# Kernel tuning notes

Hardware: AMD Instinct MI355X
Metric: run time of the kernel (lower is better)

## Reference

```python
import jax, jax.numpy as jnp
import numpy as np


def setup_inputs() -> dict:
    key = jax.random.key(0)
    ks = jax.random.split(key, 7)
    B, Q, K, H, D, R = 2, 2048, 2048, 16, 64, 32
    queries = jax.random.normal(ks[0], (B, Q, H, D), dtype=jnp.float32)
    keys = jax.random.normal(ks[1], (B, K, H, D), dtype=jnp.float32)
    values = jax.random.normal(ks[2], (B, K, H, D), dtype=jnp.float32)
    att_mask = jax.random.randint(ks[3], (B, Q, K), 0, 2, dtype=jnp.int32)
    relative_att_ids = jax.random.randint(ks[4], (B, Q, K), 0, R, dtype=jnp.int32)
    # TruncatedNormal(stddev=0.5) approximated by clipped normal
    relative_emb_table = jnp.clip(
        0.5 * jax.random.normal(ks[5], (R, H, D), dtype=jnp.float32), -1.0, 1.0)
    relative_bias_table = jnp.zeros((R, H), dtype=jnp.float32)
    return {
        'queries': queries,
        'keys': keys,
        'values': values,
        'att_mask': att_mask,
        'relative_att_ids': relative_att_ids,
        'relative_emb_table': relative_emb_table,
        'relative_bias_table': relative_bias_table,
    }


def reference(queries, keys, values, att_mask, relative_att_ids,
              relative_emb_table, relative_bias_table):
    # content scores: [B,Q,K,H]
    content = jnp.einsum('bqhd,bkhd->bqkh', queries, keys)
    # relative scores per vocab id: [B,Q,R,H]
    all_rel = jnp.einsum('bqhd,rhd->bqrh', queries, relative_emb_table)
    all_rel = all_rel + relative_bias_table  # broadcast [R,H]
    # gather along vocab axis per (q,k): [B,Q,K,H]
    rel = jnp.take_along_axis(
        all_rel, relative_att_ids[:, :, :, None].astype(jnp.int32), axis=2)
    scores = content + rel
    d = queries.shape[-1]
    scores = scores / jnp.sqrt(jnp.asarray(d, scores.dtype))
    mask_adder = -10000.0 * (1.0 - att_mask[:, :, :, None].astype(scores.dtype))
    scores = scores + mask_adder
    probs = jax.nn.softmax(scores, axis=-2)  # softmax over key axis
    return jnp.einsum('bqkh,bkhd->bqhd', probs, values)
```

## Files before the change

### kernel.cpp

```cpp
#include <hip/hip_runtime.h>
#include <hip/hip_fp16.h>
#include <stdint.h>

#define Bn 2
#define Qn 2048
#define Kn 2048
#define Hn 16
#define Dn 64
#define Rn 32

#define LOG2E_8 0.18033688011112042f
#define MASK_NEG -14426.950408889634f

typedef __attribute__((ext_vector_type(8))) short short8v;
typedef __attribute__((ext_vector_type(4))) float f32x4;
typedef __attribute__((ext_vector_type(4))) uint32_t u32x4;

static __device__ __forceinline__ uint16_t bf16rn(float f) {
  uint32_t u = __builtin_bit_cast(uint32_t, f);
  u += 0x7FFFu + ((u >> 16) & 1u);
  return (uint16_t)(u >> 16);
}
static __device__ __forceinline__ float bf16f(uint16_t h) {
  return __builtin_bit_cast(float, (uint32_t)h << 16);
}
static __device__ __forceinline__ float exp2a(float x) {
  float r; asm("v_exp_f32 %0, %1" : "=v"(r) : "v"(x)); return r;
}
static __device__ __forceinline__ uint32_t cvtpk(float lo, float hi) {
  uint32_t r; asm("v_cvt_pk_bf16_f32 %0, %1, %2" : "=v"(r) : "v"(lo), "v"(hi)); return r;
}
static __device__ __forceinline__ void gl_lds16(const void* g, void* l) {
  __builtin_amdgcn_global_load_lds((const __attribute__((address_space(1))) void*)g,
                                   (__attribute__((address_space(3))) void*)l, 16, 0, 0);
}

__global__ void pack_kernel(const int* __restrict__ ids,
                            const int* __restrict__ msk,
                            uint32_t* __restrict__ outp, int n4) {
  int i = blockIdx.x * 256 + threadIdx.x;
  if (i >= n4) return;
  int4 a = reinterpret_cast<const int4*>(ids)[i];
  int4 m = reinterpret_cast<const int4*>(msk)[i];
  uint32_t v = (uint32_t)((a.x | (m.x << 5)) & 0x3f)
             | ((uint32_t)((a.y | (m.y << 5)) & 0x3f) << 8)
             | ((uint32_t)((a.z | (m.z << 5)) & 0x3f) << 16)
             | ((uint32_t)((a.w | (m.w << 5)) & 0x3f) << 24);
  outp[i] = v;
}

__global__ __launch_bounds__(256) void kfrag6_kernel(const float* __restrict__ Kg,
                                                     const float* __restrict__ Vg,
                                                     uint8_t* __restrict__ frag) {
  const int bid = blockIdx.x;
  const int c = bid & 63;
  const int h = (bid >> 6) & 15;
  const int b = bid >> 10;
  uint8_t* panel = frag + (size_t)(b * 16 + h) * 524288u + (size_t)c * 8192u;
  uint4* kf = reinterpret_cast<uint4*>(panel);
  uint4* vf = reinterpret_cast<uint4*>(panel + 4096);
  const int tid = threadIdx.x;
  const int sdq = tid & 7, srow = (tid >> 3) & 15, stile = tid >> 7;
  const int sg = sdq & 3, sdm = sdq >> 2;
  const float* kp = Kg + ((((size_t)b * Kn) + c * 32 + stile * 16 + srow) * Hn + h) * Dn + (sdm * 32 + sg * 4);
  const float4 x0 = *reinterpret_cast<const float4*>(kp);
  const float4 x1 = *reinterpret_cast<const float4*>(kp + 16);
  const float xs0[4] = {x0.x * LOG2E_8, x0.y * LOG2E_8, x0.z * LOG2E_8, x0.w * LOG2E_8};
  const float xs1[4] = {x1.x * LOG2E_8, x1.y * LOG2E_8, x1.z * LOG2E_8, x1.w * LOG2E_8};
  uint4 uh;
  uh.x = bf16rn(xs0[0]) | ((uint32_t)bf16rn(xs0[1]) << 16);
  uh.y = bf16rn(xs0[2]) | ((uint32_t)bf16rn(xs0[3]) << 16);
  uh.z = bf16rn(xs1[0]) | ((uint32_t)bf16rn(xs1[1]) << 16);
  uh.w = bf16rn(xs1[2]) | ((uint32_t)bf16rn(xs1[3]) << 16);
  kf[(stile * 2 + sdm) * 64 + (srow + 16 * sg)] = uh;
  const int vd = tid & 63, vkq = tid >> 6;
  const float* vp = Vg + ((((size_t)b * Kn) + c * 32 + vkq * 4) * Hn + h) * Dn + vd;
  float v0[4], v1[4];
#pragma unroll
  for (int i = 0; i < 4; ++i) {
    v0[i] = vp[i * (Hn * Dn)];
    v1[i] = vp[(16 + i) * (Hn * Dn)];
  }
  uint4 uv;
  uv.x = bf16rn(v0[0]) | ((uint32_t)bf16rn(v0[1]) << 16);
  uv.y = bf16rn(v0[2]) | ((uint32_t)bf16rn(v0[3]) << 16);
  uv.z = bf16rn(v1[0]) | ((uint32_t)bf16rn(v1[1]) << 16);
  uv.w = bf16rn(v1[2]) | ((uint32_t)bf16rn(v1[3]) << 16);
  vf[(vd >> 4) * 64 + (vd & 15) + 16 * vkq] = uv;
}

__global__ __launch_bounds__(256) void tab2_kernel(const float* __restrict__ Qg,
                                                   const float* __restrict__ Eg,
                                                   const float* __restrict__ biasg,
                                                   __half* __restrict__ tabg) {
  const int tid = threadIdx.x;
  const int lane = tid & 63;
  const int w = tid >> 6;
  const int qr = lane & 15;
  const int g = lane >> 4;
  const int bid = blockIdx.x;
  const int qt = bid & 31;
  const int h = (bid >> 5) & 15;
  const int b = bid >> 9;
  const int q0 = qt * 64 + w * 16;

  short8v eh[2][2], el[2][2];
#pragma unroll
  for (int rt = 0; rt < 2; ++rt)
#pragma unroll
    for (int dm = 0; dm < 2; ++dm) {
      const float* ep = Eg + (((size_t)(rt * 16 + qr) * Hn + h) * Dn) + dm * 32 + 4 * g;
      const float4 x0 = *reinterpret_cast<const float4*>(ep);
      const float4 x1 = *reinterpret_cast<const float4*>(ep + 16);
      const float xs[8] = {x0.x * LOG2E_8, x0.y * LOG2E_8, x0.z * LOG2E_8, x0.w * LOG2E_8,
                           x1.x * LOG2E_8, x1.y * LOG2E_8, x1.z * LOG2E_8, x1.w * LOG2E_8};
#pragma unroll
      for (int j = 0; j < 8; ++j) {
        const uint16_t hi = bf16rn(xs[j]);
        eh[rt][dm][j] = (short)hi;
        el[rt][dm][j] = (short)bf16rn(xs[j] - bf16f(hi));
      }
    }
  short8v qh[2], ql[2];
#pragma unroll
  for (int dm = 0; dm < 2; ++dm) {
    const float* qp = Qg + (((size_t)b * Qn + q0 + qr) * Hn + h) * Dn + dm * 32 + 4 * g;
    const float4 x0 = *reinterpret_cast<const float4*>(qp);
    const float4 x1 = *reinterpret_cast<const float4*>(qp + 16);
    const float xs[8] = {x0.x, x0.y, x0.z, x0.w, x1.x, x1.y, x1.z, x1.w};
#pragma unroll
    for (int j = 0; j < 8; ++j) {
      const uint16_t hi = bf16rn(xs[j]);
      qh[dm][j] = (short)hi;
      ql[dm][j] = (short)bf16rn(xs[j] - bf16f(hi));
    }
  }
#pragma unroll
  for (int rt = 0; rt < 2; ++rt) {
    f32x4 d;
#pragma unroll
    for (int j = 0; j < 4; ++j)
      d[j] = LOG2E_8 * biasg[(rt * 16 + 4 * g + j) * Hn + h];
#pragma unroll
    for (int dm = 0; dm < 2; ++dm) {
      d = __builtin_amdgcn_mfma_f32_16x16x32_bf16(eh[rt][dm], qh[dm], d, 0, 0, 0);
      d = __builtin_amdgcn_mfma_f32_16x16x32_bf16(el[rt][dm], qh[dm], d, 0, 0, 0);
      d = __builtin_amdgcn_mfma_f32_16x16x32_bf16(eh[rt][dm], ql[dm], d, 0, 0, 0);
    }
    const size_t rowo = ((size_t)(b * 16 + h) * 2048 + q0 + qr) * 64;
    union { ushort4 u4; __half hh[4]; } um, uu;
#pragma unroll
    for (int j = 0; j < 4; ++j) {
      um.hh[j] = __float2half(d[j] + MASK_NEG);
      uu.hh[j] = __float2half(d[j]);
    }
    *reinterpret_cast<ushort4*>(&tabg[rowo + rt * 16 + 4 * g]) = um.u4;
    *reinterpret_cast<ushort4*>(&tabg[rowo + 32 + rt * 16 + 4 * g]) = uu.u4;
  }
}

__global__ __launch_bounds__(512, 4) void attn9_kernel(
    const float* __restrict__ Qg, const uint8_t* __restrict__ packed,
    const uint8_t* __restrict__ kfragp, const __half* __restrict__ tabg,
    float* __restrict__ outg) {
  __shared__ alignas(16) char smem[65536];
  const int tid = threadIdx.x;
  const int lane = tid & 63;
  const int w = tid >> 6;
  const int w4 = w & 3;
  const int ks = w >> 2;
  const int qr = lane & 15;
  const int g = lane >> 4;

  const int wi = (blockIdx.x & 7) * 64 + (blockIdx.x >> 3);
  const int qt = wi & 15;
  const int h = (wi >> 4) & 15;
  const int b = wi >> 8;
  const int q0 = qt * 128;

  char* const myhalf = smem + 16384 + ks * 24576;
  char* bA = myhalf;
  char* bB = myhalf + 8192;
  char* bC = myhalf + 16384;

  int64_t prow[2];
  int trow[2];
#pragma unroll
  for (int t = 0; t < 2; ++t) {
    prow[t] = ((int64_t)(b * Qn + q0 + w4 * 32 + t * 16 + qr)) * Kn + ks * 1024 + 4 * g;
    trow[t] = (w4 * 32 + t * 16 + qr) * 64;
  }
  uint32_t pc[2][2], pn[2][2] = {{0u, 0u}, {0u, 0u}};
#pragma unroll
  for (int t = 0; t < 2; ++t)
#pragma unroll
    for (int st = 0; st < 2; ++st)
      pc[t][st] = *reinterpret_cast<const uint32_t*>(packed + prow[t] + st * 16);

  {
    const uint8_t* tsrc = reinterpret_cast<const uint8_t*>(
        tabg + ((size_t)(b * 16 + h) * 2048 + q0) * 64);
    char* ld = smem + w * 2048;
    gl_lds16(tsrc + (size_t)w * 2048 + (size_t)lane * 16, ld);
    gl_lds16(tsrc + (size_t)w * 2048 + 1024 + (size_t)lane * 16, ld + 1024);
  }
  const uint8_t* sbase = kfragp + (size_t)(b * 16 + h) * 524288u +
                         (size_t)(ks * 32) * 8192u + (size_t)w4 * 2048 + (size_t)lane * 16;
  {
    char* ld0 = bA + w4 * 2048;
    gl_lds16(sbase, ld0);
    gl_lds16(sbase + 1024, ld0 + 1024);
    char* ld1 = bB + w4 * 2048;
    gl_lds16(sbase + 8192, ld1);
    gl_lds16(sbase + 8192 + 1024, ld1 + 1024);
  }

  short8v qhi[2][2];
#pragma unroll
  for (int t = 0; t < 2; ++t)
#pragma unroll
    for (int dm = 0; dm < 2; ++dm) {
      const float* qp = Qg + (((size_t)b * Qn + q0 + w4 * 32 + t * 16 + qr) * Hn + h) * Dn +
                        dm * 32 + 4 * g;
      const float4 x0 = *reinterpret_cast<const float4*>(qp);
      const float4 x1 = *reinterpret_cast<const float4*>(qp + 16);
      u32x4 u;
      u[0] = cvtpk(x0.x, x0.y); u[1] = cvtpk(x0.z, x0.w);
      u[2] = cvtpk(x1.x, x1.y); u[3] = cvtpk(x1.z, x1.w);
      qhi[t][dm] = __builtin_bit_cast(short8v, u);
    }

  asm volatile("s_waitcnt vmcnt(0)" ::: "memory");
  __builtin_amdgcn_sched_barrier(0);
  __syncthreads();

  const short8v ones = {(short)0x3F80, (short)0x3F80, (short)0x3F80, (short)0x3F80,
                        (short)0x3F80, (short)0x3F80, (short)0x3F80, (short)0x3F80};
  const __half* tabh = reinterpret_cast<const __half*>(smem);

  f32x4 acc[2][4] = {{{0.f,0.f,0.f,0.f},{0.f,0.f,0.f,0.f},{0.f,0.f,0.f,0.f},{0.f,0.f,0.f,0.f}},
                     {{0.f,0.f,0.f,0.f},{0.f,0.f,0.f,0.f},{0.f,0.f,0.f,0.f},{0.f,0.f,0.f,0.f}}};
  f32x4 accl[2] = {{0.f,0.f,0.f,0.f},{0.f,0.f,0.f,0.f}};

  for (int c = 0; c < 32; ++c) {
    if (c + 1 < 32) {
      const int64_t kb = (int64_t)(c + 1) * 32;
#pragma unroll
      for (int t = 0; t < 2; ++t)
#pragma unroll
        for (int st = 0; st < 2; ++st)
          pn[t][st] = *reinterpret_cast<const uint32_t*>(packed + prow[t] + kb + st * 16);
    }
    if (c + 2 < 32) {
      const uint8_t* gs = sbase + (size_t)(c + 2) * 8192u;
      char* ld = bC + w4 * 2048;
      gl_lds16(gs, ld);
      gl_lds16(gs + 1024, ld + 1024);
    }

    const short8v* kfs = reinterpret_cast<const short8v*>(bA);
    f32x4 s[2][2] = {{{0.f,0.f,0.f,0.f},{0.f,0.f,0.f,0.f}},
                     {{0.f,0.f,0.f,0.f},{0.f,0.f,0.f,0.f}}};
    __builtin_amdgcn_s_setprio(1);
#pragma unroll
    for (int dm = 0; dm < 2; ++dm) {
      const short8v k0 = kfs[dm * 64 + lane];
      const short8v k1 = kfs[(2 + dm) * 64 + lane];
#pragma unroll
      for (int t = 0; t < 2; ++t) {
        s[t][0] = __builtin_amdgcn_mfma_f32_16x16x32_bf16(k0, qhi[t][dm], s[t][0], 0, 0, 0);
        s[t][1] = __builtin_amdgcn_mfma_f32_16x16x32_bf16(k1, qhi[t][dm], s[t][1], 0, 0, 0);
      }
    }
    __builtin_amdgcn_s_setprio(0);

    const short8v* vfs = reinterpret_cast<const short8v*>(bA + 4096);
    short8v vv[4];
#pragma unroll
    for (int dt = 0; dt < 4; ++dt) vv[dt] = vfs[dt * 64 + lane];

#pragma unroll
    for (int t = 0; t < 2; ++t) {
      float pv[8];
#pragma unroll
      for (int i = 0; i < 8; ++i) {
        const int st = i >> 2, r = i & 3;
        const uint32_t v = (pc[t][st] >> (8 * r)) & 63u;
        pv[i] = exp2a(s[t][st][r] + __half2float(tabh[trow[t] + (int)v]));
      }
      u32x4 pu;
      pu[0] = cvtpk(pv[0], pv[1]); pu[1] = cvtpk(pv[2], pv[3]);
      pu[2] = cvtpk(pv[4], pv[5]); pu[3] = cvtpk(pv[6], pv[7]);
      const short8v pa = __builtin_bit_cast(short8v, pu);
      __builtin_amdgcn_s_setprio(1);
#pragma unroll
      for (int dt = 0; dt < 4; ++dt)
        acc[t][dt] = __builtin_amdgcn_mfma_f32_16x16x32_bf16(pa, vv[dt], acc[t][dt], 0, 0, 0);
      accl[t] = __builtin_amdgcn_mfma_f32_16x16x32_bf16(pa, ones, accl[t], 0, 0, 0);
      __builtin_amdgcn_s_setprio(0);
    }

    if (c + 1 < 32) {
#pragma unroll
      for (int t = 0; t < 2; ++t) { pc[t][0] = pn[t][0]; pc[t][1] = pn[t][1]; }
    }

    if (c < 30) {
      asm volatile("s_waitcnt vmcnt(6)" ::: "memory");
    } else {
      asm volatile("s_waitcnt vmcnt(0)" ::: "memory");
    }
    __builtin_amdgcn_sched_barrier(0);
    __syncthreads();
    char* tmp = bA; bA = bB; bB = bC; bC = tmp;
  }

  float* const acc1s = reinterpret_cast<float*>(smem + 16384);
  float* const l1s   = reinterpret_cast<float*>(smem);
  if (ks == 1) {
#pragma unroll
    for (int t = 0; t < 2; ++t) {
#pragma unroll
      for (int dt = 0; dt < 4; ++dt)
#pragma unroll
        for (int r = 0; r < 4; ++r)
          acc1s[(w4 * 32 + t * 16 + 4 * g + r) * 64 + dt * 16 + qr] = acc[t][dt][r];
#pragma unroll
      for (int r = 0; r < 4; ++r)
        l1s[w4 * 32 + t * 16 + 4 * g + r] = accl[t][r];
    }
  }
  __syncthreads();
  if (ks == 0) {
#pragma unroll
    for (int t = 0; t < 2; ++t) {
      const f32x4 l1v = *reinterpret_cast<const f32x4*>(&l1s[w4 * 32 + t * 16 + 4 * g]);
      f32x4 linv;
#pragma unroll
      for (int r = 0; r < 4; ++r) linv[r] = 1.0f / (accl[t][r] + l1v[r]);
#pragma unroll
      for (int dt = 0; dt < 4; ++dt)
#pragma unroll
        for (int r = 0; r < 4; ++r) {
          const int lrow = w4 * 32 + t * 16 + 4 * g + r;
          const float o = (acc[t][dt][r] + acc1s[lrow * 64 + dt * 16 + qr]) * linv[r];
          outg[(((size_t)b * Qn + q0 + lrow) * Hn + h) * Dn + dt * 16 + qr] = o;
        }
    }
  }
}

__global__ __launch_bounds__(256) void attn_old_kernel(
    const float* __restrict__ Qg, const float* __restrict__ Kg,
    const float* __restrict__ Vg, const int* __restrict__ maskg,
    const int* __restrict__ idsg, const float* __restrict__ Eg,
    const float* __restrict__ biasg, float* __restrict__ outg) {
  __shared__ alignas(16) char smem[34304];
  float* const allrel = reinterpret_cast<float*>(smem);
  float* const q_lds  = reinterpret_cast<float*>(smem + 8448);
  float* const et_lds = reinterpret_cast<float*>(smem + 25856);
  uint4* const kfrag  = reinterpret_cast<uint4*>(smem + 8448);
  uint4* const vfrag  = reinterpret_cast<uint4*>(smem + 16640);

  const int tid  = threadIdx.x;
  const int lane = tid & 63;
  const int w    = tid >> 6;
  const int qr   = lane & 15;
  const int g    = lane >> 4;

  const int bid = blockIdx.x;
  const int h  = bid & 15;
  const int qt = (bid >> 4) & 31;
  const int b  = bid >> 9;
  const int q0 = qt * 64;

  {
    const int row = tid >> 2, dq = (tid & 3) * 16;
    const float4* s4 =
        reinterpret_cast<const float4*>(Qg + (((b * Qn) + q0 + row) * Hn + h) * Dn + dq);
    float4* dst = reinterpret_cast<float4*>(&q_lds[row * 68 + dq]);
#pragma unroll
    for (int i = 0; i < 4; ++i) dst[i] = s4[i];
  }
  {
    const int r = tid >> 3, d0 = (tid & 7) * 8;
    const float* src = Eg + ((r * Hn + h) * Dn + d0);
#pragma unroll
    for (int i = 0; i < 8; ++i) et_lds[(d0 + i) * 33 + r] = src[i];
  }
  __syncthreads();

  const int qloc = w * 16 + qr;
  short8v qhi[2], qlo[2];
#pragma unroll
  for (int dm = 0; dm < 2; ++dm) {
#pragma unroll
    for (int j = 0; j < 8; ++j) {
      const int dl = (j < 4) ? (4 * g + j) : (16 + 4 * g + (j - 4));
      const float x = q_lds[qloc * 68 + dm * 32 + dl];
      const uint16_t hi = bf16rn(x);
      qhi[dm][j] = (short)hi;
      qlo[dm][j] = (short)bf16rn(x - bf16f(hi));
    }
  }

  {
    const int r = tid & 31, q8 = tid >> 5;
    float acc[8] = {0.f, 0.f, 0.f, 0.f, 0.f, 0.f, 0.f, 0.f};
    const float bias = biasg[r * Hn + h];
    for (int d = 0; d < 64; ++d) {
      const float e = et_lds[d * 33 + r];
#pragma unroll
      for (int i = 0; i < 8; ++i) acc[i] += e * q_lds[(q8 * 8 + i) * 68 + d];
    }
#pragma unroll
    for (int i = 0; i < 8; ++i)
      allrel[(q8 * 8 + i) * 33 + r] = 0.125f * (acc[i] + bias);
  }
  __syncthreads();

  const int sdq = tid & 7, srow = (tid >> 3) & 15, stile = tid >> 7;
  const int sg = sdq & 3, sdm = sdq >> 2;
  int koff = (((b * Kn) + stile * 16 + srow) * Hn + h) * Dn + (sdm * 32 + sg * 4);
  const int kslotH = (stile * 2 + sdm) * 64 + (srow + 16 * sg);
  const int kslotL = (4 + stile * 2 + sdm) * 64 + (srow + 16 * sg);
  const int vd = tid & 63, vkq = tid >> 6;
  int voff = (((b * Kn) + vkq * 4) * Hn + h) * Dn + vd;
  const int vslot = (vd >> 4) * 64 + (vd & 15) + 16 * vkq;

  const int qglob = q0 + qloc;
  const int prow = (b * Qn + qglob) * Kn + 4 * g;

  f32x4 acc[4] = {{0.f,0.f,0.f,0.f},{0.f,0.f,0.f,0.f},{0.f,0.f,0.f,0.f},{0.f,0.f,0.f,0.f}};
  float mrun = -1e30f, lrun = 0.f;

  const short8v* kfs = reinterpret_cast<const short8v*>(kfrag);
  const short8v* vfs = reinterpret_cast<const short8v*>(vfrag);

  for (int c = 0; c < 64; ++c) {
    const int kb = c * 32;
    __syncthreads();
    {
      const float4 x0 = *reinterpret_cast<const float4*>(Kg + koff);
      const float4 x1 = *reinterpret_cast<const float4*>(Kg + koff + 16);
      koff += 32 * Hn * Dn;
      const float xs0[4] = {x0.x, x0.y, x0.z, x0.w};
      const float xs1[4] = {x1.x, x1.y, x1.z, x1.w};
      uint16_t hh[8], ll[8];
#pragma unroll
      for (int i = 0; i < 4; ++i) {
        const uint16_t h0 = bf16rn(xs0[i]);
        const uint16_t h1 = bf16rn(xs1[i]);
        hh[i] = h0; hh[4 + i] = h1;
        ll[i] = bf16rn(xs0[i] - bf16f(h0));
        ll[4 + i] = bf16rn(xs1[i] - bf16f(h1));
      }
      uint4 uh, ul;
      uh.x = hh[0] | ((uint32_t)hh[1] << 16); uh.y = hh[2] | ((uint32_t)hh[3] << 16);
      uh.z = hh[4] | ((uint32_t)hh[5] << 16); uh.w = hh[6] | ((uint32_t)hh[7] << 16);
      ul.x = ll[0] | ((uint32_t)ll[1] << 16); ul.y = ll[2] | ((uint32_t)ll[3] << 16);
      ul.z = ll[4] | ((uint32_t)ll[5] << 16); ul.w = ll[6] | ((uint32_t)ll[7] << 16);
      kfrag[kslotH] = uh;
      kfrag[kslotL] = ul;
    }
    {
      float v0[4], v1[4];
#pragma unroll
      for (int i = 0; i < 4; ++i) {
        v0[i] = Vg[voff + i * (Hn * Dn)];
        v1[i] = Vg[voff + 16 * Hn * Dn + i * (Hn * Dn)];
      }
      voff += 32 * Hn * Dn;
      uint4 uv;
      uv.x = bf16rn(v0[0]) | ((uint32_t)bf16rn(v0[1]) << 16);
      uv.y = bf16rn(v0[2]) | ((uint32_t)bf16rn(v0[3]) << 16);
      uv.z = bf16rn(v1[0]) | ((uint32_t)bf16rn(v1[1]) << 16);
      uv.w = bf16rn(v1[2]) | ((uint32_t)bf16rn(v1[3]) << 16);
      vfrag[vslot] = uv;
    }
    __syncthreads();

    f32x4 s0 = {0.f, 0.f, 0.f, 0.f}, s1 = {0.f, 0.f, 0.f, 0.f};
#pragma unroll
    for (int dm = 0; dm < 2; ++dm) {
      const short8v k0h = kfs[(dm) * 64 + lane];
      const short8v k1h = kfs[(2 + dm) * 64 + lane];
      const short8v k0l = kfs[(4 + dm) * 64 + lane];
      const short8v k1l = kfs[(6 + dm) * 64 + lane];
      s0 = __builtin_amdgcn_mfma_f32_16x16x32_bf16(k0h, qhi[dm], s0, 0, 0, 0);
      s1 = __builtin_amdgcn_mfma_f32_16x16x32_bf16(k1h, qhi[dm], s1, 0, 0, 0);
      s0 = __builtin_amdgcn_mfma_f32_16x16x32_bf16(k0h, qlo[dm], s0, 0, 0, 0);
      s1 = __builtin_amdgcn_mfma_f32_16x16x32_bf16(k1h, qlo[dm], s1, 0, 0, 0);
      s0 = __builtin_amdgcn_mfma_f32_16x16x32_bf16(k0l, qhi[dm], s0, 0, 0, 0);
      s1 = __builtin_amdgcn_mfma_f32_16x16x32_bf16(k1l, qhi[dm], s1, 0, 0, 0);
    }

    float sv[8];
    {
      const int ib = prow + kb;
      const int4 i0 = *reinterpret_cast<const int4*>(idsg + ib);
      const int4 i1 = *reinterpret_cast<const int4*>(idsg + ib + 16);
      const int4 m0 = *reinterpret_cast<const int4*>(maskg + ib);
      const int4 m1 = *reinterpret_cast<const int4*>(maskg + ib + 16);
      const int ia0[4] = {i0.x, i0.y, i0.z, i0.w};
      const int ia1[4] = {i1.x, i1.y, i1.z, i1.w};
      const int ma0[4] = {m0.x, m0.y, m0.z, m0.w};
      const int ma1[4] = {m1.x, m1.y, m1.z, m1.w};
#pragma unroll
      for (int r = 0; r < 4; ++r) {
        sv[r]     = 0.125f * s0[r] + allrel[qloc * 33 + ia0[r]] + (ma0[r] ? 0.f : -10000.f);
        sv[4 + r] = 0.125f * s1[r] + allrel[qloc * 33 + ia1[r]] + (ma1[r] ? 0.f : -10000.f);
      }
    }

    float m8 = sv[0];
#pragma unroll
    for (int i = 1; i < 8; ++i) m8 = fmaxf(m8, sv[i]);
    m8 = fmaxf(m8, __shfl_xor(m8, 16));
    m8 = fmaxf(m8, __shfl_xor(m8, 32));
    const float mnew = fmaxf(mrun, m8);
    const float sc = __expf(mrun - mnew);
    mrun = mnew;
    float pv[8];
    float ps = 0.f;
#pragma unroll
    for (int i = 0; i < 8; ++i) { pv[i] = __expf(sv[i] - mnew); ps += pv[i]; }
    ps += __shfl_xor(ps, 16);
    ps += __shfl_xor(ps, 32);
    lrun = lrun * sc + ps;

    f32x4 scv;
#pragma unroll
    for (int r = 0; r < 4; ++r) scv[r] = __shfl(sc, 4 * g + r);
#pragma unroll
    for (int dt = 0; dt < 4; ++dt) acc[dt] *= scv;

    short8v pa;
#pragma unroll
    for (int i = 0; i < 8; ++i) pa[i] = (short)bf16rn(pv[i]);
#pragma unroll
    for (int dt = 0; dt < 4; ++dt)
      acc[dt] = __builtin_amdgcn_mfma_f32_16x16x32_bf16(pa, vfs[dt * 64 + lane], acc[dt], 0, 0, 0);
  }

  const float linv = 1.0f / lrun;
  f32x4 lv;
#pragma unroll
  for (int r = 0; r < 4; ++r) lv[r] = __shfl(linv, 4 * g + r);
#pragma unroll
  for (int dt = 0; dt < 4; ++dt) {
#pragma unroll
    for (int r = 0; r < 4; ++r) {
      const int qrow = q0 + w * 16 + 4 * g + r;
      outg[(((b * Qn) + qrow) * Hn + h) * Dn + dt * 16 + qr] = acc[dt][r] * lv[r];
    }
  }
}

extern "C" void kernel_launch(void* const* d_in, const int* in_sizes, int n_in,
                              void* d_out, int out_size, void* d_ws, size_t ws_size,
                              hipStream_t stream) {
  const float* Qg    = (const float*)d_in[0];
  const float* Kg    = (const float*)d_in[1];
  const float* Vg    = (const float*)d_in[2];
  const int*   maskg = (const int*)d_in[3];
  const int*   idsg  = (const int*)d_in[4];
  const float* Eg    = (const float*)d_in[5];
  const float* biasg = (const float*)d_in[6];
  float* outg = (float*)d_out;

  const size_t oPack = 0;
  const size_t oK    = 8388608;
  const size_t oT    = 25165824;
  const size_t need9 = 33554432;
  const int n4 = (Bn * Qn * Kn) / 4;

  uint8_t* ws = (uint8_t*)d_ws;

  if (ws_size >= need9) {
    pack_kernel<<<n4 / 256, 256, 0, stream>>>(idsg, maskg, (uint32_t*)(ws + oPack), n4);
    kfrag6_kernel<<<Bn * Hn * 64, 256, 0, stream>>>(Kg, Vg, ws + oK);
    tab2_kernel<<<Bn * Hn * 32, 256, 0, stream>>>(Qg, Eg, biasg, (__half*)(ws + oT));
    attn9_kernel<<<Bn * Hn * (Qn / 128), 512, 0, stream>>>(
        Qg, ws + oPack, ws + oK, (const __half*)(ws + oT), outg);
  } else {
    attn_old_kernel<<<Bn * Hn * (Qn / 64), 256, 0, stream>>>(
        Qg, Kg, Vg, maskg, idsg, Eg, biasg, outg);
  }
}
```

Measured before the change: 111.9 us.

## Load K/V fragments directly into registers and shrink blocks to 64 queries

The attention kernel stops staging K/V fragments in a triple-buffered LDS ring with async global-to-LDS copies and per-chunk barriers. Each wave now loads its K fragments for the next chunk straight into registers (software prefetch) and loads V fragments per chunk from global memory. Blocks shrink from 512 threads over 128 queries to 256 threads over 64 queries, with much smaller LDS, so more blocks fit per CU and the in-loop __syncthreads disappear. The trade-off is that K/V data is no longer shared across waves through LDS, so global/L2 traffic for K/V roughly doubles and register pressure rises, and V loads are not prefetched ahead of use.

```diff
diff --git a/kernel.cpp b/kernel.cpp
--- a/kernel.cpp
+++ b/kernel.cpp
@@ -159,43 +159,24 @@
   }
 }
 
-__global__ __launch_bounds__(512, 4) void attn9_kernel(
+__global__ __launch_bounds__(256, 3) void attn10_kernel(
     const float* __restrict__ Qg, const uint8_t* __restrict__ packed,
     const uint8_t* __restrict__ kfragp, const __half* __restrict__ tabg,
     float* __restrict__ outg) {
-  __shared__ alignas(16) char smem[65536];
+  __shared__ alignas(16) char smem[24832];
   const int tid = threadIdx.x;
   const int lane = tid & 63;
   const int w = tid >> 6;
-  const int w4 = w & 3;
-  const int ks = w >> 2;
+  const int wq = w & 1;
+  const int ks = w >> 1;
   const int qr = lane & 15;
   const int g = lane >> 4;
 
-  const int wi = (blockIdx.x & 7) * 64 + (blockIdx.x >> 3);
-  const int qt = wi & 15;
-  const int h = (wi >> 4) & 15;
-  const int b = wi >> 8;
-  const int q0 = qt * 128;
-
-  char* const myhalf = smem + 16384 + ks * 24576;
-  char* bA = myhalf;
-  char* bB = myhalf + 8192;
-  char* bC = myhalf + 16384;
-
-  int64_t prow[2];
-  int trow[2];
-#pragma unroll
-  for (int t = 0; t < 2; ++t) {
-    prow[t] = ((int64_t)(b * Qn + q0 + w4 * 32 + t * 16 + qr)) * Kn + ks * 1024 + 4 * g;
-    trow[t] = (w4 * 32 + t * 16 + qr) * 64;
-  }
-  uint32_t pc[2][2], pn[2][2] = {{0u, 0u}, {0u, 0u}};
-#pragma unroll
-  for (int t = 0; t < 2; ++t)
-#pragma unroll
-    for (int st = 0; st < 2; ++st)
-      pc[t][st] = *reinterpret_cast<const uint32_t*>(packed + prow[t] + st * 16);
+  const int wi = (blockIdx.x & 7) * 128 + (blockIdx.x >> 3);
+  const int qt = wi & 31;
+  const int h = (wi >> 5) & 15;
+  const int b = wi >> 9;
+  const int q0 = qt * 64;
 
   {
     const uint8_t* tsrc = reinterpret_cast<const uint8_t*>(
@@ -204,23 +185,16 @@
     gl_lds16(tsrc + (size_t)w * 2048 + (size_t)lane * 16, ld);
     gl_lds16(tsrc + (size_t)w * 2048 + 1024 + (size_t)lane * 16, ld + 1024);
   }
-  const uint8_t* sbase = kfragp + (size_t)(b * 16 + h) * 524288u +
-                         (size_t)(ks * 32) * 8192u + (size_t)w4 * 2048 + (size_t)lane * 16;
-  {
-    char* ld0 = bA + w4 * 2048;
-    gl_lds16(sbase, ld0);
-    gl_lds16(sbase + 1024, ld0 + 1024);
-    char* ld1 = bB + w4 * 2048;
-    gl_lds16(sbase + 8192, ld1);
-    gl_lds16(sbase + 8192 + 1024, ld1 + 1024);
-  }
+
+  const uint8_t* panel = kfragp + (size_t)(b * 16 + h) * 524288u + (size_t)(ks * 32) * 8192u +
+                         (size_t)lane * 16;
 
   short8v qhi[2][2];
 #pragma unroll
   for (int t = 0; t < 2; ++t)
 #pragma unroll
     for (int dm = 0; dm < 2; ++dm) {
-      const float* qp = Qg + (((size_t)b * Qn + q0 + w4 * 32 + t * 16 + qr) * Hn + h) * Dn +
+      const float* qp = Qg + (((size_t)b * Qn + q0 + wq * 32 + t * 16 + qr) * Hn + h) * Dn +
                         dm * 32 + 4 * g;
       const float4 x0 = *reinterpret_cast<const float4*>(qp);
       const float4 x1 = *reinterpret_cast<const float4*>(qp + 16);
@@ -230,6 +204,25 @@
       qhi[t][dm] = __builtin_bit_cast(short8v, u);
     }
 
+  int64_t prow[2];
+  int trow[2];
+#pragma unroll
+  for (int t = 0; t < 2; ++t) {
+    prow[t] = ((int64_t)(b * Qn + q0 + wq * 32 + t * 16 + qr)) * Kn + ks * 1024 + 4 * g;
+    trow[t] = (wq * 32 + t * 16 + qr) * 64;
+  }
+  uint32_t pc[2][2], pn[2][2] = {{0u, 0u}, {0u, 0u}};
+#pragma unroll
+  for (int t = 0; t < 2; ++t)
+#pragma unroll
+    for (int st = 0; st < 2; ++st)
+      pc[t][st] = *reinterpret_cast<const uint32_t*>(packed + prow[t] + st * 16);
+
+  short8v kc[4], kn[4];
+#pragma unroll
+  for (int s = 0; s < 4; ++s)
+    kc[s] = *reinterpret_cast<const short8v*>(panel + s * 1024);
+
   asm volatile("s_waitcnt vmcnt(0)" ::: "memory");
   __builtin_amdgcn_sched_barrier(0);
   __syncthreads();
@@ -244,6 +237,10 @@
 
   for (int c = 0; c < 32; ++c) {
     if (c + 1 < 32) {
+      const uint8_t* pnx = panel + (size_t)(c + 1) * 8192u;
+#pragma unroll
+      for (int s = 0; s < 4; ++s)
+        kn[s] = *reinterpret_cast<const short8v*>(pnx + s * 1024);
       const int64_t kb = (int64_t)(c + 1) * 32;
 #pragma unroll
       for (int t = 0; t < 2; ++t)
@@ -251,21 +248,21 @@
         for (int st = 0; st < 2; ++st)
           pn[t][st] = *reinterpret_cast<const uint32_t*>(packed + prow[t] + kb + st * 16);
     }
-    if (c + 2 < 32) {
-      const uint8_t* gs = sbase + (size_t)(c + 2) * 8192u;
-      char* ld = bC + w4 * 2048;
-      gl_lds16(gs, ld);
-      gl_lds16(gs + 1024, ld + 1024);
-    }
-
-    const short8v* kfs = reinterpret_cast<const short8v*>(bA);
+    short8v vv[4];
+    {
+      const uint8_t* pv4 = panel + (size_t)c * 8192u + 4096;
+#pragma unroll
+      for (int dt = 0; dt < 4; ++dt)
+        vv[dt] = *reinterpret_cast<const short8v*>(pv4 + dt * 1024);
+    }
+
     f32x4 s[2][2] = {{{0.f,0.f,0.f,0.f},{0.f,0.f,0.f,0.f}},
                      {{0.f,0.f,0.f,0.f},{0.f,0.f,0.f,0.f}}};
     __builtin_amdgcn_s_setprio(1);
 #pragma unroll
     for (int dm = 0; dm < 2; ++dm) {
-      const short8v k0 = kfs[dm * 64 + lane];
-      const short8v k1 = kfs[(2 + dm) * 64 + lane];
+      const short8v k0 = kc[dm];
+      const short8v k1 = kc[2 + dm];
 #pragma unroll
       for (int t = 0; t < 2; ++t) {
         s[t][0] = __builtin_amdgcn_mfma_f32_16x16x32_bf16(k0, qhi[t][dm], s[t][0], 0, 0, 0);
@@ -273,11 +270,6 @@
       }
     }
     __builtin_amdgcn_s_setprio(0);
-
-    const short8v* vfs = reinterpret_cast<const short8v*>(bA + 4096);
-    short8v vv[4];
-#pragma unroll
-    for (int dt = 0; dt < 4; ++dt) vv[dt] = vfs[dt * 64 + lane];
 
 #pragma unroll
     for (int t = 0; t < 2; ++t) {
@@ -300,23 +292,14 @@
       __builtin_amdgcn_s_setprio(0);
     }
 
-    if (c + 1 < 32) {
-#pragma unroll
-      for (int t = 0; t < 2; ++t) { pc[t][0] = pn[t][0]; pc[t][1] = pn[t][1]; }
-    }
-
-    if (c < 30) {
-      asm volatile("s_waitcnt vmcnt(6)" ::: "memory");
-    } else {
-      asm volatile("s_waitcnt vmcnt(0)" ::: "memory");
-    }
-    __builtin_amdgcn_sched_barrier(0);
-    __syncthreads();
-    char* tmp = bA; bA = bB; bB = bC; bC = tmp;
-  }
-
-  float* const acc1s = reinterpret_cast<float*>(smem + 16384);
-  float* const l1s   = reinterpret_cast<float*>(smem);
+#pragma unroll
+    for (int s4i = 0; s4i < 4; ++s4i) kc[s4i] = kn[s4i];
+#pragma unroll
+    for (int t = 0; t < 2; ++t) { pc[t][0] = pn[t][0]; pc[t][1] = pn[t][1]; }
+  }
+
+  float* const acc1s = reinterpret_cast<float*>(smem + 8192);
+  float* const l1s   = reinterpret_cast<float*>(smem + 24576);
   if (ks == 1) {
 #pragma unroll
     for (int t = 0; t < 2; ++t) {
@@ -324,17 +307,17 @@
       for (int dt = 0; dt < 4; ++dt)
 #pragma unroll
         for (int r = 0; r < 4; ++r)
-          acc1s[(w4 * 32 + t * 16 + 4 * g + r) * 64 + dt * 16 + qr] = acc[t][dt][r];
+          acc1s[(wq * 32 + t * 16 + 4 * g + r) * 64 + dt * 16 + qr] = acc[t][dt][r];
 #pragma unroll
       for (int r = 0; r < 4; ++r)
-        l1s[w4 * 32 + t * 16 + 4 * g + r] = accl[t][r];
+        l1s[wq * 32 + t * 16 + 4 * g + r] = accl[t][r];
     }
   }
   __syncthreads();
   if (ks == 0) {
 #pragma unroll
     for (int t = 0; t < 2; ++t) {
-      const f32x4 l1v = *reinterpret_cast<const f32x4*>(&l1s[w4 * 32 + t * 16 + 4 * g]);
+      const f32x4 l1v = *reinterpret_cast<const f32x4*>(&l1s[wq * 32 + t * 16 + 4 * g]);
       f32x4 linv;
 #pragma unroll
       for (int r = 0; r < 4; ++r) linv[r] = 1.0f / (accl[t][r] + l1v[r]);
@@ -342,7 +325,7 @@
       for (int dt = 0; dt < 4; ++dt)
 #pragma unroll
         for (int r = 0; r < 4; ++r) {
-          const int lrow = w4 * 32 + t * 16 + 4 * g + r;
+          const int lrow = wq * 32 + t * 16 + 4 * g + r;
           const float o = (acc[t][dt][r] + acc1s[lrow * 64 + dt * 16 + qr]) * linv[r];
           outg[(((size_t)b * Qn + q0 + lrow) * Hn + h) * Dn + dt * 16 + qr] = o;
         }
@@ -572,16 +555,16 @@
   const size_t oPack = 0;
   const size_t oK    = 8388608;
   const size_t oT    = 25165824;
-  const size_t need9 = 33554432;
+  const size_t need10 = 33554432;
   const int n4 = (Bn * Qn * Kn) / 4;
 
   uint8_t* ws = (uint8_t*)d_ws;
 
-  if (ws_size >= need9) {
+  if (ws_size >= need10) {
     pack_kernel<<<n4 / 256, 256, 0, stream>>>(idsg, maskg, (uint32_t*)(ws + oPack), n4);
     kfrag6_kernel<<<Bn * Hn * 64, 256, 0, stream>>>(Kg, Vg, ws + oK);
     tab2_kernel<<<Bn * Hn * 32, 256, 0, stream>>>(Qg, Eg, biasg, (__half*)(ws + oT));
-    attn9_kernel<<<Bn * Hn * (Qn / 128), 512, 0, stream>>>(
+    attn10_kernel<<<Bn * Hn * (Qn / 64), 256, 0, stream>>>(
         Qg, ws + oPack, ws + oK, (const __half*)(ws + oT), outg);
   } else {
     attn_old_kernel<<<Bn * Hn * (Qn / 64), 256, 0, stream>>>(
```

Measured after the change: 130.3 us. +16.4%, slower.
